# Kernel optimization log

Measured on AMD Instinct MI355X. Metric: run time of the kernel, lower is better.

Reference implementation:

```python
import jax, jax.numpy as jnp
import numpy as np

NX = 96      # polar grid size (nx x nx)
NETA = 96    # cartesian grid size (neta x neta)
B = 64       # batch


def _rotation_index(n):
    # Static permutation: nx copies of the flat index grid, each rolled by (-i,-i).
    idx = np.arange(n * n).reshape(n, n)
    return np.concatenate([np.roll(idx, shift=(-i, -i), axis=(0, 1)) for i in range(n)], axis=0)  # [n*n, n]


def setup_inputs() -> dict:
    key = jax.random.key(0)
    ks = jax.random.split(key, 18)
    f = lambda k, s: jax.random.normal(k, s, dtype=jnp.float32) * 0.05
    inp = {
        "inputs": f(ks[0], (B, 2, NX * NX)),
        "cart_mat": f(ks[1], (NETA * NETA, NX * NX)),
    }
    for i, name in enumerate(["pre1", "pre2", "pre3", "pre4", "post1", "post2", "post3", "post4"]):
        inp[name] = f(ks[2 + i], (1, NX))
    for i, name in enumerate(["cos_kernel1", "sin_kernel1", "cos_kernel2", "sin_kernel2",
                              "cos_kernel3", "sin_kernel3", "cos_kernel4", "sin_kernel4"]):
        inp[name] = f(ks[10 + i], (NX, NX))
    return inp


def reference(inputs, cart_mat, pre1, pre2, pre3, pre4, post1, post2, post3, post4,
              cos_kernel1, sin_kernel1, cos_kernel2, sin_kernel2,
              cos_kernel3, sin_kernel3, cos_kernel4, sin_kernel4):
    nx, neta = NX, NETA
    ridx = jnp.asarray(_rotation_index(nx).reshape(-1))  # [nx^3] static gather indices
    R, I = inputs[:, 0, :], inputs[:, 1, :]              # each [B, nx^2]
    # Rotation-index gather (vectorized over batch), -> [B*nx, nx, nx]
    Rs = jnp.take(R, ridx, axis=1).reshape(-1, nx, nx)
    Is = jnp.take(I, ridx, axis=1).reshape(-1, nx, nx)

    def helper(pre, post, kernel2, kernel1, data):
        # post @ (kernel2 * ((data * pre) @ kernel1)) : [B*nx, 1, nx]
        return jnp.matmul(post, kernel2 * jnp.matmul(data * pre, kernel1))

    output_polar = (helper(pre1, post1, cos_kernel1, cos_kernel2, Rs)
                    + helper(pre2, post2, sin_kernel1, sin_kernel2, Rs)
                    + helper(pre3, post3, cos_kernel3, sin_kernel3, Is)
                    + helper(pre4, post4, sin_kernel4, cos_kernel4, Is))  # [B*nx, 1, nx]
    output_polar = output_polar.reshape(-1, nx * nx)  # [B, nx^2]
    # Batched polar->cartesian: cart_mat @ x per sample == x @ cart_mat.T
    output_cart = jnp.einsum('bn,mn->bm', output_polar, cart_mat)  # [B, neta^2]
    return output_cart.reshape(-1, neta, neta, 1)
```

## Files before the change

kernel.cpp:

```cpp
#include <hip/hip_runtime.h>

typedef __bf16 bf16x8 __attribute__((ext_vector_type(8)));
typedef float floatx4 __attribute__((ext_vector_type(4)));
typedef unsigned int u32;
typedef unsigned short u16;

__device__ __forceinline__ u16 f2bf_bits(float f) {
  __bf16 h = (__bf16)f;
  return __builtin_bit_cast(u16, h);
}

__global__ __launch_bounds__(256) void k_prep(
    const float* __restrict__ pre1, const float* __restrict__ pre2,
    const float* __restrict__ pre3, const float* __restrict__ pre4,
    const float* __restrict__ post1, const float* __restrict__ post2,
    const float* __restrict__ post3, const float* __restrict__ post4,
    const float* __restrict__ ck1, const float* __restrict__ sk1,
    const float* __restrict__ ck2, const float* __restrict__ sk2,
    const float* __restrict__ ck3, const float* __restrict__ sk3,
    const float* __restrict__ ck4, const float* __restrict__ sk4,
    float* __restrict__ Pf, u16* __restrict__ Qbf)
{
  int idx = blockIdx.x * 256 + threadIdx.x;
  int h = idx / 9216;
  int rem = idx - h * 9216;
  int y = rem / 96;
  int z = rem - y * 96;
  const float* pre  = (h == 0) ? pre1 : (h == 1) ? pre2 : (h == 2) ? pre3 : pre4;
  const float* post = (h == 0) ? post1 : (h == 1) ? post2 : (h == 2) ? post3 : post4;
  const float* K1   = (h == 0) ? ck2 : (h == 1) ? sk2 : (h == 2) ? sk3 : ck4;
  const float* K2   = (h == 0) ? ck1 : (h == 1) ? sk1 : (h == 2) ? ck3 : sk4;
  Pf[idx] = pre[y] * K1[y * 96 + z];
  Qbf[h * 9216 + z * 96 + y] = f2bf_bits(post[y] * K2[y * 96 + z]);
}

template<int IR>
__device__ __forceinline__ uint4 shift_frag(uint4 lo, uint4 hi) {
  u32 s[8] = {lo.x, lo.y, lo.z, lo.w, hi.x, hi.y, hi.z, hi.w};
  uint4 o;
  constexpr int m = IR >> 1;
  if constexpr ((IR & 1) == 0) {
    o.x = s[m + 0]; o.y = s[m + 1]; o.z = s[m + 2]; o.w = s[m + 3];
  } else {
    o.x = (s[m + 0] >> 16) | (s[m + 1] << 16);
    o.y = (s[m + 1] >> 16) | (s[m + 2] << 16);
    o.z = (s[m + 2] >> 16) | (s[m + 3] << 16);
    o.w = (s[m + 3] >> 16) | (s[m + 4] << 16);
  }
  return o;
}

__device__ __forceinline__ void shift3(const uint4* lo, const uint4* hi, int ir, uint4* out) {
  switch (ir) {
    case 0: out[0]=shift_frag<0>(lo[0],hi[0]); out[1]=shift_frag<0>(lo[1],hi[1]); out[2]=shift_frag<0>(lo[2],hi[2]); break;
    case 1: out[0]=shift_frag<1>(lo[0],hi[0]); out[1]=shift_frag<1>(lo[1],hi[1]); out[2]=shift_frag<1>(lo[2],hi[2]); break;
    case 2: out[0]=shift_frag<2>(lo[0],hi[0]); out[1]=shift_frag<2>(lo[1],hi[1]); out[2]=shift_frag<2>(lo[2],hi[2]); break;
    case 3: out[0]=shift_frag<3>(lo[0],hi[0]); out[1]=shift_frag<3>(lo[1],hi[1]); out[2]=shift_frag<3>(lo[2],hi[2]); break;
    case 4: out[0]=shift_frag<4>(lo[0],hi[0]); out[1]=shift_frag<4>(lo[1],hi[1]); out[2]=shift_frag<4>(lo[2],hi[2]); break;
    case 5: out[0]=shift_frag<5>(lo[0],hi[0]); out[1]=shift_frag<5>(lo[1],hi[1]); out[2]=shift_frag<5>(lo[2],hi[2]); break;
    case 6: out[0]=shift_frag<6>(lo[0],hi[0]); out[1]=shift_frag<6>(lo[1],hi[1]); out[2]=shift_frag<6>(lo[2],hi[2]); break;
    default:out[0]=shift_frag<7>(lo[0],hi[0]); out[1]=shift_frag<7>(lo[1],hi[1]); out[2]=shift_frag<7>(lo[2],hi[2]); break;
  }
}

__global__ __launch_bounds__(256, 2) void k_stage1(
    const float* __restrict__ inputs,
    const u16* __restrict__ Qbf,
    const float* __restrict__ Pf,
    u16* __restrict__ polar)
{
  __shared__ __align__(16) u16 Xd[96 * 128];
  __shared__ float pacc[6][96];

  int blk = blockIdx.x;
  int b = blk >> 4;
  int i0 = (blk & 15) * 6;
  int W = 8 * (i0 >> 3);
  int tid = threadIdx.x;
  int lane = tid & 63;
  int w = tid >> 6;
  int l15 = lane & 15;
  int lg = lane >> 4;
  int chalf = w >> 1;
  int nhalf = w & 1;

  for (int e = tid; e < 576; e += 256) ((float*)pacc)[e] = 0.f;

  for (int ph = 0; ph < 2; ++ph) {
    __syncthreads();
    const float4* src4 = reinterpret_cast<const float4*>(
        inputs + (size_t)b * 18432 + ph * 9216);
    for (int e4 = tid; e4 < 2304; e4 += 256) {
      int rX = e4 / 24;
      int kq = e4 - rX * 24;
      float4 v = src4[e4];
      int c = rX - W; if (c < 0) c += 96;
      int ch = c >> 3, cs = c & 7;
      int c2 = c + 96;
      int ch2 = c2 >> 3, cs2 = c2 & 7;
      bool dup = (c < 16);
#pragma unroll
      for (int j = 0; j < 4; ++j) {
        int row = kq * 4 + j;
        u16 bv = f2bf_bits(((const float*)&v)[j]);
        int sw = row & 7;
        Xd[row * 128 + ((ch ^ sw) << 3) + cs] = bv;
        if (dup) Xd[row * 128 + ((ch2 ^ sw) << 3) + cs2] = bv;
      }
    }
    __syncthreads();

    bf16x8 Qf[2][3][3];
#pragma unroll
    for (int h2 = 0; h2 < 2; ++h2)
#pragma unroll
      for (int ct = 0; ct < 3; ++ct)
#pragma unroll
        for (int ks = 0; ks < 3; ++ks)
          Qf[h2][ct][ks] = *reinterpret_cast<const bf16x8*>(
              Qbf + (ph * 2 + h2) * 9216 +
              (chalf * 48 + ct * 16 + l15) * 96 + ks * 32 + lg * 8);

    for (int ii = 0; ii < 6; ++ii) {
      int i = i0 + ii;
      int s = i - W;
      int ia = s >> 3, ir = s & 7;
      floatx4 svc[3];
      svc[0] = 0.f; svc[1] = 0.f; svc[2] = 0.f;

      for (int ntl = 0; ntl < 3; ++ntl) {
        int nt = nhalf * 3 + ntl;
        int row = nt * 16 + l15;
        const u16* xr = &Xd[row * 128];
        int sw = row & 7;
        uint4 lo[3], hi[3];
#pragma unroll
        for (int ks = 0; ks < 3; ++ks) {
          int chE = ks * 4 + lg + ia;
          lo[ks] = *reinterpret_cast<const uint4*>(xr + (((chE    ) ^ sw) << 3));
          hi[ks] = *reinterpret_cast<const uint4*>(xr + (((chE + 1) ^ sw) << 3));
        }
        uint4 Bu[3];
        shift3(lo, hi, ir, Bu);

        floatx4 acc[2][3];
#pragma unroll
        for (int h2 = 0; h2 < 2; ++h2)
#pragma unroll
          for (int ct = 0; ct < 3; ++ct) acc[h2][ct] = 0.f;

#pragma unroll
        for (int ks = 0; ks < 3; ++ks) {
          bf16x8 bb = __builtin_bit_cast(bf16x8, Bu[ks]);
#pragma unroll
          for (int h2 = 0; h2 < 2; ++h2)
#pragma unroll
            for (int ct = 0; ct < 3; ++ct)
              acc[h2][ct] = __builtin_amdgcn_mfma_f32_16x16x32_bf16(
                  Qf[h2][ct][ks], bb, acc[h2][ct], 0, 0, 0);
        }

        int krot = nt * 16 + l15 - i; if (krot < 0) krot += 96;
#pragma unroll
        for (int h2 = 0; h2 < 2; ++h2) {
          const float* PfH = Pf + (ph * 2 + h2) * 9216 + krot * 96 + chalf * 48;
#pragma unroll
          for (int ct = 0; ct < 3; ++ct) {
            floatx4 pw = *reinterpret_cast<const floatx4*>(PfH + ct * 16 + lg * 4);
            svc[ct] += pw * acc[h2][ct];
          }
        }
      }

#pragma unroll
      for (int ct = 0; ct < 3; ++ct) {
        int c0 = chalf * 48 + ct * 16 + lg * 4;
#pragma unroll
        for (int q = 0; q < 4; ++q) {
          float v = svc[ct][q];
          v += __shfl_xor(v, 1);
          v += __shfl_xor(v, 2);
          v += __shfl_xor(v, 4);
          v += __shfl_xor(v, 8);
          if (l15 == 0) atomicAdd(&pacc[ii][c0 + q], v);
        }
      }
    }
  }

  __syncthreads();
  for (int e = tid; e < 576; e += 256) {
    int ii = e / 96;
    int c = e - ii * 96;
    polar[(size_t)b * 9216 + (i0 + ii) * 96 + c] = f2bf_bits(pacc[ii][c]);
  }
}

__global__ __launch_bounds__(256) void k_stage2(
    const u16* __restrict__ polar,
    const float* __restrict__ cart,
    float* __restrict__ part)
{
  int tid = threadIdx.x;
  int lane = tid & 63;
  int w = tid >> 6;
  int l15 = lane & 15;
  int m = blockIdx.x * 64 + w * 16 + l15;
  int kg = (lane >> 4) * 8;
  int k0 = blockIdx.y * 576;

  floatx4 acc[4] = {};

  const float* crow = cart + (size_t)m * 9216 + k0 + kg;
  const u16* prow = polar + (size_t)l15 * 9216 + k0 + kg;

  for (int ks = 0; ks < 18; ++ks) {
    floatx4 c0 = *reinterpret_cast<const floatx4*>(crow);
    floatx4 c1 = *reinterpret_cast<const floatx4*>(crow + 4);
    bf16x8 bf;
    bf[0] = (__bf16)c0[0]; bf[1] = (__bf16)c0[1]; bf[2] = (__bf16)c0[2]; bf[3] = (__bf16)c0[3];
    bf[4] = (__bf16)c1[0]; bf[5] = (__bf16)c1[1]; bf[6] = (__bf16)c1[2]; bf[7] = (__bf16)c1[3];
#pragma unroll
    for (int bt = 0; bt < 4; ++bt) {
      bf16x8 af = *reinterpret_cast<const bf16x8*>(prow + bt * 147456);
      acc[bt] = __builtin_amdgcn_mfma_f32_16x16x32_bf16(af, bf, acc[bt], 0, 0, 0);
    }
    crow += 32;
    prow += 32;
  }

  int rg = (lane >> 4) * 4;
#pragma unroll
  for (int bt = 0; bt < 4; ++bt) {
    int b0 = bt * 16 + rg;
#pragma unroll
    for (int q = 0; q < 4; ++q) {
      part[((size_t)blockIdx.y * 64 + b0 + q) * 9216 + m] = acc[bt][q];
    }
  }
}

__global__ __launch_bounds__(256) void k_reduce(
    const float* __restrict__ part, float* __restrict__ out)
{
  int idx = blockIdx.x * 256 + threadIdx.x;
  float s = 0.f;
#pragma unroll
  for (int sp = 0; sp < 16; ++sp) s += part[(size_t)sp * 589824 + idx];
  out[idx] = s;
}

extern "C" void kernel_launch(void* const* d_in, const int* in_sizes, int n_in,
                              void* d_out, int out_size, void* d_ws, size_t ws_size,
                              hipStream_t stream) {
  const float* inputs = (const float*)d_in[0];
  const float* cart   = (const float*)d_in[1];

  char* ws = (char*)d_ws;
  float* Pf   = (float*)(ws + 0);
  u16*   Qbf  = (u16*)(ws + 147456);
  u16*   polar= (u16*)(ws + 221184);
  float* part = (float*)(ws + 1400832);

  k_prep<<<144, 256, 0, stream>>>(
      (const float*)d_in[2],  (const float*)d_in[3],  (const float*)d_in[4],  (const float*)d_in[5],
      (const float*)d_in[6],  (const float*)d_in[7],  (const float*)d_in[8],  (const float*)d_in[9],
      (const float*)d_in[10], (const float*)d_in[11], (const float*)d_in[12], (const float*)d_in[13],
      (const float*)d_in[14], (const float*)d_in[15], (const float*)d_in[16], (const float*)d_in[17],
      Pf, Qbf);

  k_stage1<<<1024, 256, 0, stream>>>(inputs, Qbf, Pf, polar);

  k_stage2<<<dim3(144, 16), 256, 0, stream>>>(polar, cart, part);

  k_reduce<<<2304, 256, 0, stream>>>(part, (float*)d_out);
}
```

Baseline: 669.9 us.

## Restructure stage1 loops to keep per-row accumulators in registers, drop LDS atomics

```diff
diff --git a/kernel.cpp b/kernel.cpp
--- a/kernel.cpp
+++ b/kernel.cpp
@@ -8,6 +8,10 @@
 __device__ __forceinline__ u16 f2bf_bits(float f) {
   __bf16 h = (__bf16)f;
   return __builtin_bit_cast(u16, h);
+}
+
+__device__ __forceinline__ void keep4(uint4& v) {
+  asm("" : "+v"(v.x), "+v"(v.y), "+v"(v.z), "+v"(v.w));
 }
 
 __global__ __launch_bounds__(256) void k_prep(
@@ -70,12 +74,13 @@
     u16* __restrict__ polar)
 {
   __shared__ __align__(16) u16 Xd[96 * 128];
-  __shared__ float pacc[6][96];
+  __shared__ float pacc[2][6][96];
 
   int blk = blockIdx.x;
   int b = blk >> 4;
   int i0 = (blk & 15) * 6;
   int W = 8 * (i0 >> 3);
+  int s0 = i0 - W;
   int tid = threadIdx.x;
   int lane = tid & 63;
   int w = tid >> 6;
@@ -84,7 +89,11 @@
   int chalf = w >> 1;
   int nhalf = w & 1;
 
-  for (int e = tid; e < 576; e += 256) ((float*)pacc)[e] = 0.f;
+  float svc[6][3];
+#pragma unroll
+  for (int ii = 0; ii < 6; ++ii)
+#pragma unroll
+    for (int ct = 0; ct < 3; ++ct) svc[ii][ct] = 0.f;
 
   for (int ph = 0; ph < 2; ++ph) {
     __syncthreads();
@@ -116,23 +125,35 @@
 #pragma unroll
       for (int ct = 0; ct < 3; ++ct)
 #pragma unroll
-        for (int ks = 0; ks < 3; ++ks)
-          Qf[h2][ct][ks] = *reinterpret_cast<const bf16x8*>(
+        for (int ks = 0; ks < 3; ++ks) {
+          uint4 t = *reinterpret_cast<const uint4*>(
               Qbf + (ph * 2 + h2) * 9216 +
               (chalf * 48 + ct * 16 + l15) * 96 + ks * 32 + lg * 8);
-
-    for (int ii = 0; ii < 6; ++ii) {
-      int i = i0 + ii;
-      int s = i - W;
-      int ia = s >> 3, ir = s & 7;
-      floatx4 svc[3];
-      svc[0] = 0.f; svc[1] = 0.f; svc[2] = 0.f;
-
-      for (int ntl = 0; ntl < 3; ++ntl) {
-        int nt = nhalf * 3 + ntl;
-        int row = nt * 16 + l15;
-        const u16* xr = &Xd[row * 128];
-        int sw = row & 7;
+          keep4(t);
+          Qf[h2][ct][ks] = __builtin_bit_cast(bf16x8, t);
+        }
+
+    for (int ntl = 0; ntl < 3; ++ntl) {
+      int nt = nhalf * 3 + ntl;
+      float pw[2][3][4];
+#pragma unroll
+      for (int h2 = 0; h2 < 2; ++h2)
+#pragma unroll
+        for (int ct = 0; ct < 3; ++ct)
+#pragma unroll
+          for (int q = 0; q < 4; ++q)
+            pw[h2][ct][q] = Pf[(ph * 2 + h2) * 9216 +
+                               (nt * 16 + lg * 4 + q) * 96 +
+                               chalf * 48 + ct * 16 + l15];
+      int rowb = nt * 16 + l15 + i0;
+
+#pragma unroll
+      for (int ii = 0; ii < 6; ++ii) {
+        int s = s0 + ii;
+        int ia = s >> 3, ir = s & 7;
+        int rowIdx = rowb + ii; if (rowIdx >= 96) rowIdx -= 96;
+        const u16* xr = &Xd[rowIdx * 128];
+        int sw = rowIdx & 7;
         uint4 lo[3], hi[3];
 #pragma unroll
         for (int ks = 0; ks < 3; ++ks) {
@@ -151,48 +172,43 @@
 
 #pragma unroll
         for (int ks = 0; ks < 3; ++ks) {
-          bf16x8 bb = __builtin_bit_cast(bf16x8, Bu[ks]);
+          bf16x8 aa = __builtin_bit_cast(bf16x8, Bu[ks]);
 #pragma unroll
           for (int h2 = 0; h2 < 2; ++h2)
 #pragma unroll
             for (int ct = 0; ct < 3; ++ct)
               acc[h2][ct] = __builtin_amdgcn_mfma_f32_16x16x32_bf16(
-                  Qf[h2][ct][ks], bb, acc[h2][ct], 0, 0, 0);
+                  aa, Qf[h2][ct][ks], acc[h2][ct], 0, 0, 0);
         }
 
-        int krot = nt * 16 + l15 - i; if (krot < 0) krot += 96;
-#pragma unroll
-        for (int h2 = 0; h2 < 2; ++h2) {
-          const float* PfH = Pf + (ph * 2 + h2) * 9216 + krot * 96 + chalf * 48;
-#pragma unroll
-          for (int ct = 0; ct < 3; ++ct) {
-            floatx4 pw = *reinterpret_cast<const floatx4*>(PfH + ct * 16 + lg * 4);
-            svc[ct] += pw * acc[h2][ct];
-          }
-        }
+#pragma unroll
+        for (int h2 = 0; h2 < 2; ++h2)
+#pragma unroll
+          for (int ct = 0; ct < 3; ++ct)
+            svc[ii][ct] += pw[h2][ct][0] * acc[h2][ct][0]
+                         + pw[h2][ct][1] * acc[h2][ct][1]
+                         + pw[h2][ct][2] * acc[h2][ct][2]
+                         + pw[h2][ct][3] * acc[h2][ct][3];
       }
-
-#pragma unroll
-      for (int ct = 0; ct < 3; ++ct) {
-        int c0 = chalf * 48 + ct * 16 + lg * 4;
-#pragma unroll
-        for (int q = 0; q < 4; ++q) {
-          float v = svc[ct][q];
-          v += __shfl_xor(v, 1);
-          v += __shfl_xor(v, 2);
-          v += __shfl_xor(v, 4);
-          v += __shfl_xor(v, 8);
-          if (l15 == 0) atomicAdd(&pacc[ii][c0 + q], v);
-        }
-      }
-    }
-  }
+    }
+  }
+
+#pragma unroll
+  for (int ii = 0; ii < 6; ++ii)
+#pragma unroll
+    for (int ct = 0; ct < 3; ++ct) {
+      float v = svc[ii][ct];
+      v += __shfl_xor(v, 16);
+      v += __shfl_xor(v, 32);
+      if (lg == 0) pacc[nhalf][ii][chalf * 48 + ct * 16 + l15] = v;
+    }
 
   __syncthreads();
   for (int e = tid; e < 576; e += 256) {
     int ii = e / 96;
     int c = e - ii * 96;
-    polar[(size_t)b * 9216 + (i0 + ii) * 96 + c] = f2bf_bits(pacc[ii][c]);
+    polar[(size_t)b * 9216 + (i0 + ii) * 96 + c] =
+        f2bf_bits(pacc[0][ii][c] + pacc[1][ii][c]);
   }
 }
 
```

After: 659.3 us. About the same (-1.6%).
